# Kernel optimization log

Hardware: AMD Instinct MI355X
Metric: run time of the kernel (lower is better)

Reference implementation:

```python
import jax, jax.numpy as jnp
import numpy as np

CONF_THRESH = 0.01
TOP_K = 200
NMS_THRESH = 0.45


def decode(loc, dbox):
    # loc, dbox: [N,4]; dbox is (cx, cy, w, h)
    cxcy = dbox[:, :2] + loc[:, :2] * 0.1 * dbox[:, 2:]
    wh = dbox[:, 2:] * jnp.exp(loc[:, 2:] * 0.2)
    xymin = cxcy - wh * 0.5
    xymax = xymin + wh
    return jnp.concatenate([xymin, xymax], axis=1)  # [N,4] (x1,y1,x2,y2)


def nms_class(scores, boxes):
    # scores: [N], boxes: [N,4]. Mirrors torch greedy NMS with fixed-size padding.
    masked = jnp.where(scores > CONF_THRESH, scores, -1.0)
    topv, topi = jax.lax.top_k(masked, TOP_K)  # descending score, like idx[-top_k:] reversed
    cb = boxes[topi]  # [K,4]
    valid = topv > CONF_THRESH
    x1, y1, x2, y2 = cb[:, 0], cb[:, 1], cb[:, 2], cb[:, 3]
    area = (x2 - x1) * (y2 - y1)
    ar = jnp.arange(TOP_K)

    def body(i, keep):
        cur = keep[i]
        w = jnp.clip(jnp.minimum(x2, x2[i]) - jnp.maximum(x1, x1[i]), 0.0)
        h = jnp.clip(jnp.minimum(y2, y2[i]) - jnp.maximum(y1, y1[i]), 0.0)
        inter = w * h
        iou = inter / (area - inter + area[i])  # union = rem_area - inter + area[i]
        sup = (iou > NMS_THRESH) & (ar > i) & cur
        return keep & (~sup)

    keep = jax.lax.fori_loop(0, TOP_K, body, valid)
    # compact kept rows to the front, preserving descending-score order (stable sort)
    order = jnp.argsort(jnp.logical_not(keep), stable=True)
    count = jnp.sum(keep)
    rows = jnp.concatenate([topv[:, None], cb], axis=1)[order]  # [K,5] = (score, x1,y1,x2,y2)
    return jnp.where(ar[:, None] < count, rows, 0.0)


def setup_inputs() -> dict:
    key = jax.random.key(0)
    k1, k2, k3, k4 = jax.random.split(key, 4)
    B, N, C = 128, 8732, 21
    loc_data = jax.random.normal(k1, (B, N, 4), dtype=jnp.float32) * 0.5
    conf_data = jax.random.normal(k2, (B, N, C), dtype=jnp.float32)
    centers = jax.random.uniform(k3, (N, 2), dtype=jnp.float32)
    wh = jax.random.uniform(k4, (N, 2), dtype=jnp.float32, minval=0.02, maxval=0.3)
    dbox_list = jnp.concatenate([centers, wh], axis=1)
    return {"loc_data": loc_data, "conf_data": conf_data, "dbox_list": dbox_list}


def reference(loc_data, conf_data, dbox_list):
    conf = jax.nn.softmax(conf_data, axis=-1)                              # [B,N,C]
    boxes = jax.vmap(decode, in_axes=(0, None))(loc_data, dbox_list)       # [B,N,4]
    # vmap over classes (axis 1 of per-image conf) then over batch
    per_cls = jax.vmap(jax.vmap(nms_class, in_axes=(1, None)),
                       in_axes=(0, 0))(conf, boxes)                        # [B,C,K,5]
    return per_cls.at[:, 0].set(0.0)  # class 0 (background) is skipped in torch
```

## Files before the change

kernel.cpp:

```cpp
#include <hip/hip_runtime.h>

#define N_ANCH 8732
#define NCLS   21
#define BATCH  128
#define TOPK   200
#define CONF_T 0.01f
#define NMS_T  0.45f
#define HSIZE  1024
#define CAND_MAX 1024
#define NQ4    2183

__device__ __forceinline__ float exp_np(float x) {
    const float fx = floorf(__fmaf_rn(x, 1.442695040888963f, 0.5f));
    float t = __fmaf_rn(fx, -0.693359375f, x);
    t = __fmaf_rn(fx, 2.12194440e-4f, t);
    const float z = __fmul_rn(t, t);
    float y = 1.9875691500e-4f;
    y = __fmaf_rn(y, t, 1.3981999507e-3f);
    y = __fmaf_rn(y, t, 8.3334519073e-3f);
    y = __fmaf_rn(y, t, 4.1665795894e-2f);
    y = __fmaf_rn(y, t, 1.6666665459e-1f);
    y = __fmaf_rn(y, t, 5.0000001201e-1f);
    y = __fmaf_rn(y, z, t);
    y = __fadd_rn(y, 1.0f);
    return ldexpf(y, (int)fx);
}

__global__ __launch_bounds__(256) void prep_kernel(
    const float* __restrict__ loc, const float* __restrict__ conf,
    const float* __restrict__ dbox, float* __restrict__ probs,
    float* __restrict__ boxes)
{
    __shared__ float srow[256 * NCLS];
    const int block_row0 = blockIdx.x * 256;
    const float* cbase = conf + (size_t)block_row0 * NCLS;
    for (int i = threadIdx.x; i < 256 * NCLS; i += 256) srow[i] = cbase[i];
    __syncthreads();

    const int row = block_row0 + threadIdx.x;
    const int b = row / N_ANCH;
    const int n = row - b * N_ANCH;

    float e[NCLS];
    float m = srow[threadIdx.x * NCLS];
#pragma unroll
    for (int c = 1; c < NCLS; ++c) m = fmaxf(m, srow[threadIdx.x * NCLS + c]);
#pragma unroll
    for (int c = 0; c < NCLS; ++c)
        e[c] = exp_np(__fsub_rn(srow[threadIdx.x * NCLS + c], m));

    float acc[16];
#pragma unroll
    for (int j = 0; j < 16; ++j) acc[j] = e[j];
#pragma unroll
    for (int j = 0; j < 5; ++j) acc[j] = __fadd_rn(acc[j], e[16 + j]);
    float u[8];
#pragma unroll
    for (int j = 0; j < 8; ++j) u[j] = __fadd_rn(acc[j], acc[j + 8]);
    const float v0 = __fadd_rn(u[0], u[4]), v1 = __fadd_rn(u[1], u[5]);
    const float v2 = __fadd_rn(u[2], u[6]), v3 = __fadd_rn(u[3], u[7]);
    const float w0 = __fadd_rn(v0, v2), w1 = __fadd_rn(v1, v3);
    const float s  = __fadd_rn(w0, w1);

#pragma unroll
    for (int c = 1; c < NCLS; ++c)
        probs[((size_t)b * 20 + (c - 1)) * N_ANCH + n] = __fdiv_rn(e[c], s);

    const float4 l = *(const float4*)(loc + (size_t)row * 4);
    const float4 d = *(const float4*)(dbox + (size_t)n * 4);
    const float cx = __fmaf_rn(__fmul_rn(l.x, 0.1f), d.z, d.x);
    const float cy = __fmaf_rn(__fmul_rn(l.y, 0.1f), d.w, d.y);
    const float w  = __fmul_rn(d.z, exp_np(__fmul_rn(l.z, 0.2f)));
    const float h  = __fmul_rn(d.w, exp_np(__fmul_rn(l.w, 0.2f)));
    const float x1 = __fmaf_rn(w, -0.5f, cx);
    const float y1 = __fmaf_rn(h, -0.5f, cy);
    float4 o; o.x = x1; o.y = y1; o.z = __fadd_rn(x1, w); o.w = __fadd_rn(y1, h);
    *(float4*)(boxes + (size_t)row * 4) = o;
}

__global__ __launch_bounds__(256) void sel_kernel(
    const float* __restrict__ probs, const float* __restrict__ boxes,
    float* __restrict__ probs_mut)
{
    const int task = blockIdx.x;
    const int b = task / NCLS;
    const int c = task - b * NCLS;
    const int tid = threadIdx.x;
    if (c == 0) return;

    const float* prow = probs + ((size_t)b * 20 + (c - 1)) * N_ANCH;

    __shared__ int hist2[HSIZE * 2];
    __shared__ int wsum[4];
    __shared__ unsigned long long cand[CAND_MAX];
    __shared__ int selB;
    __shared__ int cnts[2];
    __shared__ unsigned ck[TOPK];
    __shared__ int  cn[TOPK];
    __shared__ unsigned sk[TOPK];
    __shared__ int  sn_[TOPK];

    const int wid = tid >> 6, lane = tid & 63;
    const int par = wid & 1;

    for (int i = tid; i < HSIZE * 2; i += 256) hist2[i] = 0;
    __syncthreads();
    for (int idx = tid; idx < NQ4; idx += 256) {
        const float4 v = *(const float4*)(prow + idx * 4);
        if (v.x > CONF_T) atomicAdd(&hist2[(int)((__float_as_uint(v.x) >> 16) - 0x3C23u) * 2 + par], 1);
        if (v.y > CONF_T) atomicAdd(&hist2[(int)((__float_as_uint(v.y) >> 16) - 0x3C23u) * 2 + par], 1);
        if (v.z > CONF_T) atomicAdd(&hist2[(int)((__float_as_uint(v.z) >> 16) - 0x3C23u) * 2 + par], 1);
        if (v.w > CONF_T) atomicAdd(&hist2[(int)((__float_as_uint(v.w) >> 16) - 0x3C23u) * 2 + par], 1);
    }
    __syncthreads();

    const int hbase = HSIZE - 4 * (tid + 1);
    int hb[4];
#pragma unroll
    for (int j = 0; j < 4; ++j) hb[j] = hist2[(hbase + j) * 2] + hist2[(hbase + j) * 2 + 1];
    const int part = hb[0] + hb[1] + hb[2] + hb[3];

    int incl = part;
#pragma unroll
    for (int off = 1; off < 64; off <<= 1) {
        const int v = __shfl_up(incl, off);
        if (lane >= off) incl += v;
    }
    if (lane == 63) wsum[wid] = incl;
    __syncthreads();
    int pre = 0;
    for (int w = 0; w < wid; ++w) pre += wsum[w];
    const int excl  = pre + incl - part;
    const int total = wsum[0] + wsum[1] + wsum[2] + wsum[3];
    if (tid == 0 && total < TOPK) selB = -1;
    if (excl < TOPK && excl + part >= TOPK) {
        int cacc = excl;
        for (int j = 3; j >= 0; --j) {
            if (cacc + hb[j] >= TOPK) { selB = hbase + j; break; }
            cacc += hb[j];
        }
    }
    if (tid == 0) { cnts[0] = 0; cnts[1] = 0; }
    __syncthreads();
    const int B = selB;

    for (int idx = tid; idx < NQ4; idx += 256) {
        const float4 v = *(const float4*)(prow + idx * 4);
        const float vv[4] = {v.x, v.y, v.z, v.w};
#pragma unroll
        for (int q = 0; q < 4; ++q) {
            const float s = vv[q];
            if (s > CONF_T) {
                const unsigned kk = __float_as_uint(s);
                const int bkt = (int)((kk >> 16) - 0x3C23u);
                if (bkt > B) {
                    const int p = atomicAdd(&cnts[0], 1);
                    ck[p] = kk; cn[p] = idx * 4 + q;
                } else if (bkt == B) {
                    const int qq = atomicAdd(&cnts[1], 1);
                    if (qq < CAND_MAX)
                        cand[qq] = ((unsigned long long)kk << 32) | (unsigned)(~(idx * 4 + q));
                }
            }
        }
    }
    __syncthreads();
    const int ndef  = cnts[0];
    const int slots = TOPK - ndef;
    int cc = cnts[1]; if (cc > CAND_MAX) cc = CAND_MAX;
    for (int i = tid; i < cc; i += 256) {
        const unsigned long long mine = cand[i];
        int rank = 0;
        for (int j = 0; j < cc; ++j) rank += (cand[j] > mine) ? 1 : 0;
        if (rank < slots) {
            const int p = atomicAdd(&cnts[0], 1);
            ck[p] = (unsigned)(mine >> 32);
            cn[p] = (int)(~(unsigned)mine);
        }
    }
    __syncthreads();
    const int cnt_arr = cnts[0];

    if (tid < TOPK) { sk[tid] = 0u; sn_[tid] = -1; }
    __syncthreads();
    if (tid < cnt_arr) {
        const unsigned mk = ck[tid];
        const int mn = cn[tid];
        int rank = 0;
        for (int j = 0; j < cnt_arr; ++j) {
            const unsigned kj = ck[j];
            rank += (kj > mk || (kj == mk && cn[j] < mn)) ? 1 : 0;
        }
        sk[rank] = mk; sn_[rank] = mn;
    }
    __syncthreads();

    float* selrow = probs_mut + ((size_t)b * 20 + (c - 1)) * N_ANCH;
    for (int i = tid; i < TOPK; i += 256) {
        const int n = sn_[i];
        float scv = 0.f;
        float4 bx = make_float4(0.f, 0.f, 0.f, 0.f);
        if (n >= 0) {
            scv = __uint_as_float(sk[i]);
            bx = *(const float4*)(boxes + ((size_t)b * N_ANCH + n) * 4);
        }
        float* dst = selrow + i * 5;
        dst[0] = scv; dst[1] = bx.x; dst[2] = bx.y; dst[3] = bx.z; dst[4] = bx.w;
    }
}

__global__ __launch_bounds__(256) void nms_kernel(
    const float* __restrict__ sel, float* __restrict__ out)
{
    const int task = blockIdx.x;
    const int b = task / NCLS;
    const int c = task - b * NCLS;
    float* obase = out + (size_t)task * (TOPK * 5);
    const int tid = threadIdx.x;
    const int wv = tid >> 6, lane = tid & 63;

    if (c == 0) {
        for (int i = tid; i < TOPK * 5; i += 256) obase[i] = 0.f;
        return;
    }
    const float* srow = sel + ((size_t)b * 20 + (c - 1)) * N_ANCH;

    __shared__ float bxs[TOPK * 5];
    __shared__ unsigned long long rows[TOPK][4];
    __shared__ unsigned long long Ksh[4];

    for (int i = tid; i < TOPK * 5; i += 256) bxs[i] = srow[i];
    __syncthreads();

    float jx1[4], jy1[4], jx2[4], jy2[4], jar[4];
    int jval[4];
#pragma unroll
    for (int s = 0; s < 4; ++s) {
        const int j = s * 64 + lane;
        float a = 0.f, p1 = 0.f, p2 = 0.f, p3 = 0.f, p4 = 0.f;
        if (j < TOPK) {
            a = bxs[j * 5 + 0];
            p1 = bxs[j * 5 + 1]; p2 = bxs[j * 5 + 2];
            p3 = bxs[j * 5 + 3]; p4 = bxs[j * 5 + 4];
        }
        jx1[s] = p1; jy1[s] = p2; jx2[s] = p3; jy2[s] = p4;
        jar[s] = __fmul_rn(__fsub_rn(p3, p1), __fsub_rn(p4, p2));
        jval[s] = (a > CONF_T) ? 1 : 0;
    }
    if (wv == 0) {
#pragma unroll
        for (int s = 0; s < 4; ++s) {
            const unsigned long long m = __ballot(jval[s] != 0);
            if (lane == 0) Ksh[s] = m;
        }
    }

    for (int i = wv; i < TOPK; i += 4) {
        const int smin = i >> 6;
        const float ix1 = bxs[i * 5 + 1], iy1 = bxs[i * 5 + 2];
        const float ix2 = bxs[i * 5 + 3], iy2 = bxs[i * 5 + 4];
        const float ia  = __fmul_rn(__fsub_rn(ix2, ix1), __fsub_rn(iy2, iy1));
#pragma unroll
        for (int s = 0; s < 4; ++s) {
            if (s < smin) {
                if (lane == 0) rows[i][s] = 0ull;
            } else {
                const int j = s * 64 + lane;
                const float w = fmaxf(0.f, __fsub_rn(fminf(jx2[s], ix2), fmaxf(jx1[s], ix1)));
                const float h = fmaxf(0.f, __fsub_rn(fminf(jy2[s], iy2), fmaxf(jy1[s], iy1)));
                const float inter = __fmul_rn(w, h);
                const float denom = __fadd_rn(__fsub_rn(jar[s], inter), ia);
                const float iou = __fdiv_rn(inter, denom);
                const bool bit = (j < TOPK) && (j > i) && (iou > NMS_T);
                const unsigned long long m = __ballot(bit);
                if (lane == 0) rows[i][s] = m;
            }
        }
    }
    __syncthreads();

    if (wv == 0) {
        unsigned long long K0 = Ksh[0], K1 = Ksh[1], K2 = Ksh[2], K3 = Ksh[3];
#pragma unroll
        for (int w4 = 0; w4 < 4; ++w4) {
            const int lim = (w4 < 3) ? 64 : (TOPK - 192);
            for (int o = 0; o < lim; ++o) {
                const int i = w4 * 64 + o;
                const unsigned long long r0 = rows[i][0], r1 = rows[i][1];
                const unsigned long long r2 = rows[i][2], r3 = rows[i][3];
                if ((r0 | r1 | r2 | r3) == 0ull) continue;
                unsigned long long live;
                if (w4 == 0) live = (K0 >> o) & 1ull;
                else if (w4 == 1) live = (K1 >> o) & 1ull;
                else if (w4 == 2) live = (K2 >> o) & 1ull;
                else live = (K3 >> o) & 1ull;
                const unsigned long long msel = 0ull - live;
                K0 &= ~(r0 & msel);
                K1 &= ~(r1 & msel);
                K2 &= ~(r2 & msel);
                K3 &= ~(r3 & msel);
            }
        }
        if (lane == 0) { Ksh[0] = K0; Ksh[1] = K1; Ksh[2] = K2; Ksh[3] = K3; }
    }
    __syncthreads();

    if (tid < TOPK) {
        const unsigned long long K0 = Ksh[0], K1 = Ksh[1], K2 = Ksh[2], K3 = Ksh[3];
        const int d = tid;
        const int c0 = (int)__popcll(K0), c1 = (int)__popcll(K1),
                  c2 = (int)__popcll(K2), c3 = (int)__popcll(K3);
        const int totalk = c0 + c1 + c2 + c3;
        float o0 = 0.f, o1 = 0.f, o2 = 0.f, o3 = 0.f, o4 = 0.f;
        if (d < totalk) {
            int r = d;
            unsigned long long x;
            int wbase;
            if (r < c0)               { x = K0; wbase = 0;   }
            else if (r < c0 + c1)     { x = K1; wbase = 64;  r -= c0; }
            else if (r < c0 + c1 + c2){ x = K2; wbase = 128; r -= c0 + c1; }
            else                      { x = K3; wbase = 192; r -= c0 + c1 + c2; }
            for (int t = 0; t < r; ++t) x &= x - 1ull;
            const int p = wbase + (__ffsll((unsigned long long)x) - 1);
            o0 = bxs[p * 5 + 0]; o1 = bxs[p * 5 + 1]; o2 = bxs[p * 5 + 2];
            o3 = bxs[p * 5 + 3]; o4 = bxs[p * 5 + 4];
        }
        obase[d * 5 + 0] = o0;
        obase[d * 5 + 1] = o1;
        obase[d * 5 + 2] = o2;
        obase[d * 5 + 3] = o3;
        obase[d * 5 + 4] = o4;
    }
}

extern "C" void kernel_launch(void* const* d_in, const int* in_sizes, int n_in,
                              void* d_out, int out_size, void* d_ws, size_t ws_size,
                              hipStream_t stream) {
    (void)in_sizes; (void)n_in; (void)out_size; (void)ws_size;
    const float* loc  = (const float*)d_in[0];
    const float* conf = (const float*)d_in[1];
    const float* dbox = (const float*)d_in[2];
    float* out   = (float*)d_out;
    float* probs = (float*)d_ws;
    float* boxes = (float*)((char*)d_ws + (size_t)BATCH * 20 * N_ANCH * 4);

    prep_kernel<<<(BATCH * N_ANCH) / 256, 256, 0, stream>>>(loc, conf, dbox, probs, boxes);
    sel_kernel<<<BATCH * NCLS, 256, 0, stream>>>(probs, boxes, probs);
    nms_kernel<<<BATCH * NCLS, 256, 0, stream>>>(probs, out);
}
```

Before: 222.9 us.

## Refine top-k boundary bucket via sub-histogram and replace IoU divide with compare

```diff
diff --git a/kernel.cpp b/kernel.cpp
--- a/kernel.cpp
+++ b/kernel.cpp
@@ -5,10 +5,11 @@
 #define BATCH  128
 #define TOPK   200
 #define CONF_T 0.01f
-#define NMS_T  0.45f
 #define HSIZE  1024
 #define CAND_MAX 1024
 #define NQ4    2183
+
+#define MD 0x1.CCCCCDp-2
 
 __device__ __forceinline__ float exp_np(float x) {
     const float fx = floorf(__fmaf_rn(x, 1.442695040888963f, 0.5f));
@@ -168,17 +169,64 @@
     const int ndef  = cnts[0];
     const int slots = TOPK - ndef;
     int cc = cnts[1]; if (cc > CAND_MAX) cc = CAND_MAX;
-    for (int i = tid; i < cc; i += 256) {
-        const unsigned long long mine = cand[i];
-        int rank = 0;
-        for (int j = 0; j < cc; ++j) rank += (cand[j] > mine) ? 1 : 0;
-        if (rank < slots) {
+
+    if (cc <= slots) {
+        for (int i = tid; i < cc; i += 256) {
+            const unsigned long long mine = cand[i];
             const int p = atomicAdd(&cnts[0], 1);
             ck[p] = (unsigned)(mine >> 32);
             cn[p] = (int)(~(unsigned)mine);
         }
-    }
-    __syncthreads();
+        __syncthreads();
+    } else {
+        for (int i = tid; i < 256; i += 256) hist2[i] = 0;
+        __syncthreads();
+        for (int i = tid; i < cc; i += 256)
+            atomicAdd(&hist2[(int)((cand[i] >> 40) & 0xFFull)], 1);
+        __syncthreads();
+        const int sb = 255 - tid;
+        const int part2 = hist2[sb];
+        int incl2 = part2;
+#pragma unroll
+        for (int off = 1; off < 64; off <<= 1) {
+            const int v = __shfl_up(incl2, off);
+            if (lane >= off) incl2 += v;
+        }
+        if (lane == 63) wsum[wid] = incl2;
+        __syncthreads();
+        int pre2 = 0;
+        for (int w = 0; w < wid; ++w) pre2 += wsum[w];
+        const int excl2 = pre2 + incl2 - part2;
+        if (excl2 < slots && excl2 + part2 >= slots) selB = sb;
+        __syncthreads();
+        const int B2 = selB;
+        for (int i = tid; i < cc; i += 256) {
+            const unsigned long long mine = cand[i];
+            if ((int)((mine >> 40) & 0xFFull) > B2) {
+                const int p = atomicAdd(&cnts[0], 1);
+                ck[p] = (unsigned)(mine >> 32);
+                cn[p] = (int)(~(unsigned)mine);
+            }
+        }
+        __syncthreads();
+        const int slots2 = TOPK - cnts[0];
+        for (int i = tid; i < cc; i += 256) {
+            const unsigned long long mine = cand[i];
+            if ((int)((mine >> 40) & 0xFFull) == B2) {
+                int rank = 0;
+                for (int j = 0; j < cc; ++j) {
+                    const unsigned long long oth = cand[j];
+                    rank += (((int)((oth >> 40) & 0xFFull) == B2) && oth > mine) ? 1 : 0;
+                }
+                if (rank < slots2) {
+                    const int p = atomicAdd(&cnts[0], 1);
+                    ck[p] = (unsigned)(mine >> 32);
+                    cn[p] = (int)(~(unsigned)mine);
+                }
+            }
+        }
+        __syncthreads();
+    }
     const int cnt_arr = cnts[0];
 
     if (tid < TOPK) { sk[tid] = 0u; sn_[tid] = -1; }
@@ -226,7 +274,7 @@
     const float* srow = sel + ((size_t)b * 20 + (c - 1)) * N_ANCH;
 
     __shared__ float bxs[TOPK * 5];
-    __shared__ unsigned long long rows[TOPK][4];
+    __shared__ __align__(16) unsigned long long rows[TOPK][4];
     __shared__ unsigned long long Ksh[4];
 
     for (int i = tid; i < TOPK * 5; i += 256) bxs[i] = srow[i];
@@ -270,8 +318,8 @@
                 const float h = fmaxf(0.f, __fsub_rn(fminf(jy2[s], iy2), fmaxf(jy1[s], iy1)));
                 const float inter = __fmul_rn(w, h);
                 const float denom = __fadd_rn(__fsub_rn(jar[s], inter), ia);
-                const float iou = __fdiv_rn(inter, denom);
-                const bool bit = (j < TOPK) && (j > i) && (iou > NMS_T);
+                const bool bit = (j < TOPK) && (j > i) &&
+                                 ((double)inter > MD * (double)denom);
                 const unsigned long long m = __ballot(bit);
                 if (lane == 0) rows[i][s] = m;
             }
@@ -286,19 +334,19 @@
             const int lim = (w4 < 3) ? 64 : (TOPK - 192);
             for (int o = 0; o < lim; ++o) {
                 const int i = w4 * 64 + o;
-                const unsigned long long r0 = rows[i][0], r1 = rows[i][1];
-                const unsigned long long r2 = rows[i][2], r3 = rows[i][3];
-                if ((r0 | r1 | r2 | r3) == 0ull) continue;
+                const ulonglong2 ra = *(const ulonglong2*)&rows[i][0];
+                const ulonglong2 rb = *(const ulonglong2*)&rows[i][2];
+                if ((ra.x | ra.y | rb.x | rb.y) == 0ull) continue;
                 unsigned long long live;
                 if (w4 == 0) live = (K0 >> o) & 1ull;
                 else if (w4 == 1) live = (K1 >> o) & 1ull;
                 else if (w4 == 2) live = (K2 >> o) & 1ull;
                 else live = (K3 >> o) & 1ull;
                 const unsigned long long msel = 0ull - live;
-                K0 &= ~(r0 & msel);
-                K1 &= ~(r1 & msel);
-                K2 &= ~(r2 & msel);
-                K3 &= ~(r3 & msel);
+                K0 &= ~(ra.x & msel);
+                K1 &= ~(ra.y & msel);
+                K2 &= ~(rb.x & msel);
+                K3 &= ~(rb.y & msel);
             }
         }
         if (lane == 0) { Ksh[0] = K0; Ksh[1] = K1; Ksh[2] = K2; Ksh[3] = K3; }
```

Measured after the change: 210.9 us. 1.06x faster.
